# Kernel optimization log

Measured on AMD Instinct MI355X. Metric: run time of the kernel, lower is better.

The kernel has to match this reference:

```python
import jax, jax.numpy as jnp
import numpy as np

RES = 0.16      # config.resolution (m)
XMIN = -51.2    # config.x_min
YMIN = -51.2    # config.y_min
EPS = 1e-5      # BatchNorm eps
NEG = -1.0e9


def setup_inputs() -> dict:
    key = jax.random.key(0)
    ks = jax.random.split(key, 12)
    P, M = 100000, 32
    C_IN, C_MID, C_OUT = 9, 64, 64
    pillars = jax.random.normal(ks[0], (P, M, 4), dtype=jnp.float32)
    pillar_coords = jax.random.randint(ks[1], (P, 2), 0, 640, dtype=jnp.int64)
    num_points_per_pillar = jax.random.randint(ks[2], (P,), 0, 33, dtype=jnp.int64)
    # MLP params (Linear stored as (in,out) for x @ W + b)
    W1 = jax.random.normal(ks[3], (C_IN, C_MID), dtype=jnp.float32) / np.sqrt(C_IN)
    b1 = jax.random.normal(ks[4], (C_MID,), dtype=jnp.float32) * 0.01
    g1 = jnp.ones((C_MID,), jnp.float32)
    beta1 = jnp.zeros((C_MID,), jnp.float32)
    m1 = jax.random.normal(ks[5], (C_MID,), dtype=jnp.float32) * 0.1
    v1 = jax.random.uniform(ks[6], (C_MID,), dtype=jnp.float32, minval=0.5, maxval=1.5)
    W2 = jax.random.normal(ks[7], (C_MID, C_OUT), dtype=jnp.float32) / np.sqrt(C_MID)
    b2 = jax.random.normal(ks[8], (C_OUT,), dtype=jnp.float32) * 0.01
    g2 = jnp.ones((C_OUT,), jnp.float32)
    beta2 = jnp.zeros((C_OUT,), jnp.float32)
    m2 = jax.random.normal(ks[9], (C_OUT,), dtype=jnp.float32) * 0.1
    v2 = jax.random.uniform(ks[10], (C_OUT,), dtype=jnp.float32, minval=0.5, maxval=1.5)
    return {
        "pillars": pillars, "pillar_coords": pillar_coords,
        "num_points_per_pillar": num_points_per_pillar,
        "W1": W1, "b1": b1, "g1": g1, "beta1": beta1, "m1": m1, "v1": v1,
        "W2": W2, "b2": b2, "g2": g2, "beta2": beta2, "m2": m2, "v2": v2,
    }


def reference(pillars, pillar_coords, num_points_per_pillar,
              W1, b1, g1, beta1, m1, v1, W2, b2, g2, beta2, m2, v2):
    P, M, _ = pillars.shape
    # pillar centers from grid indices
    xc = (pillar_coords[:, 1].astype(jnp.float32) + 0.5) * RES + XMIN  # (P,)
    yc = (pillar_coords[:, 0].astype(jnp.float32) + 0.5) * RES + YMIN  # (P,)
    npts = num_points_per_pillar.astype(jnp.float32)
    mask = (jnp.arange(M)[None, :] < num_points_per_pillar[:, None]).astype(pillars.dtype)  # (P,M)
    x, y, z, r = pillars[:, :, 0], pillars[:, :, 1], pillars[:, :, 2], pillars[:, :, 3]
    z_mean = (z * mask).sum(axis=1) / jnp.clip(npts, 1.0)  # (P,)
    xo = x - xc[:, None]
    yo = y - yc[:, None]
    zo = z - z_mean[:, None]
    feat = jnp.stack([x, y, z, r, xo, yo, zo, xo, yo], axis=-1)  # (P,M,9)
    # shared MLP: Linear -> BN(eval) -> ReLU, twice
    h = feat @ W1 + b1
    h = jax.nn.relu(g1 * (h - m1) * jax.lax.rsqrt(v1 + EPS) + beta1)
    h = h @ W2 + b2
    h = jax.nn.relu(g2 * (h - m2) * jax.lax.rsqrt(v2 + EPS) + beta2)  # (P,M,64)
    # masked max over points per pillar
    m3 = mask[:, :, None]
    h = h * m3 + (1.0 - m3) * NEG
    return h.max(axis=1)  # (P,64)
```

## Files before the change

kernel.cpp:

```cpp
#include <hip/hip_runtime.h>
#include <type_traits>

#define RES_ 0.16f
#define XMIN_ -51.2f
#define YMIN_ -51.2f
#define EPS_ 1e-5f
#define NEG_ -1000000000.0f

#define WPB 4

typedef _Float16 f16x8 __attribute__((ext_vector_type(8)));
typedef _Float16 f16x4 __attribute__((ext_vector_type(4)));
typedef _Float16 f16x2 __attribute__((ext_vector_type(2)));
typedef float f32x4 __attribute__((ext_vector_type(4)));

union F8u { f16x8 v; f16x2 h[4]; };
union F4u { f16x4 v; f16x2 h[2]; };

#if __has_builtin(__builtin_amdgcn_mfma_f32_16x16x16f16)
#define MFMA1_K16 1
#else
#define MFMA1_K16 0
#endif

static __device__ __forceinline__ f16x2 pkrtz(float a, float b) {
    return __builtin_bit_cast(f16x2, __builtin_amdgcn_cvt_pkrtz(a, b));
}

static __device__ __forceinline__ f16x2 relu2(f16x2 x) {
#if __has_builtin(__builtin_elementwise_max)
    const f16x2 z2 = (f16x2)(_Float16)0.f;
    return __builtin_elementwise_max(x, z2);
#else
    f16x2 r;
    r[0] = x[0] > (_Float16)0.f ? x[0] : (_Float16)0.f;
    r[1] = x[1] > (_Float16)0.f ? x[1] : (_Float16)0.f;
    return r;
#endif
}

__global__ __launch_bounds__(256, 4) void pfn_kernel(
    const float* __restrict__ pillars,
    const int* __restrict__ coords,
    const int* __restrict__ npts_arr,
    const float* __restrict__ W1, const float* __restrict__ b1,
    const float* __restrict__ g1, const float* __restrict__ beta1,
    const float* __restrict__ m1, const float* __restrict__ v1,
    const float* __restrict__ W2, const float* __restrict__ b2,
    const float* __restrict__ g2, const float* __restrict__ beta2,
    const float* __restrict__ m2, const float* __restrict__ v2,
    float* __restrict__ out, int P)
{
    __shared__ float pts[WPB][32][4];
    __shared__ __align__(16) _Float16 h1s[WPB][32][72];

    const int tid  = threadIdx.x;
    const int wave = tid >> 6;
    const int lane = tid & 63;
    const int quad = lane >> 4;
    const int col  = lane & 15;

    float c1v[4], w16v[4];
#if MFMA1_K16
    f16x4 bw1[4];
#else
    f16x8 bw1[4];
#endif
#pragma unroll
    for (int nt = 0; nt < 4; ++nt) {
        const int n0 = nt * 16 + col;
        const float a1 = g1[n0] * rsqrtf(v1[n0] + EPS_);
        c1v[nt]  = fmaf(a1, b1[n0] - m1[n0], beta1[n0]);
        w16v[nt] = a1 * W1[6 * 64 + n0];
#if MFMA1_K16
#pragma unroll
        for (int j = 0; j < 4; ++j) {
            const int k = quad * 4 + j;
            bw1[nt][j] = (k < 9) ? (_Float16)(a1 * W1[k * 64 + n0]) : (_Float16)0.f;
        }
#else
#pragma unroll
        for (int j = 0; j < 8; ++j) {
            const int k = quad * 8 + j;
            bw1[nt][j] = (k < 9) ? (_Float16)(a1 * W1[k * 64 + n0]) : (_Float16)0.f;
        }
#endif
    }

    f16x8 bw2[2][4];
#pragma unroll
    for (int nt = 0; nt < 4; ++nt) {
        const int n0 = nt * 16 + col;
        const float a2 = g2[n0] * rsqrtf(v2[n0] + EPS_);
#pragma unroll
        for (int kt = 0; kt < 2; ++kt)
#pragma unroll
            for (int j = 0; j < 8; ++j) {
                const int phys = kt * 32 + quad * 8 + j;
                const int orig = (phys & 3) * 16 + (phys >> 2);
                bw2[kt][nt][j] = (_Float16)(a2 * W2[orig * 64 + n0]);
            }
    }
    const float a2o   = g2[lane] * rsqrtf(v2[lane] + EPS_);
    const float c2own = fmaf(a2o, b2[lane] - m2[lane], beta2[lane]);

    const int nwaves = gridDim.x * WPB;
    int p = __builtin_amdgcn_readfirstlane(blockIdx.x * WPB + wave);
    if (p >= P) return;

    float2 pv = ((const float2*)(pillars + (size_t)p * 128))[lane];
    int np = npts_arr[p];
    int cy = coords[2 * p], cx = coords[2 * p + 1];

    while (true) {
        const int pn = p + nwaves;
        const bool has_next = pn < P;
        float2 pvn; int npn = 0, cyn = 0, cxn = 0;
        if (has_next) {
            pvn = ((const float2*)(pillars + (size_t)pn * 128))[lane];
            npn = npts_arr[pn];
            cyn = coords[2 * pn]; cxn = coords[2 * pn + 1];
        }

        np = np < 0 ? 0 : (np > 32 ? 32 : np);
        const int npu = __builtin_amdgcn_readfirstlane(np);
        const float xc = ((float)cx + 0.5f) * RES_ + XMIN_;
        const float yc = ((float)cy + 0.5f) * RES_ + YMIN_;

        ((float2*)&pts[wave][0][0])[lane] = pv;

        float zv = ((lane & 1) && ((lane >> 1) < np)) ? pv.x : 0.0f;
#pragma unroll
        for (int off = 1; off <= 32; off <<= 1) zv += __shfl_xor(zv, off, 64);
        const float z_mean = zv / fmaxf((float)np, 1.0f);

        __threadfence_block();

        auto body = [&](auto MTC) -> float {
            constexpr int MT = decltype(MTC)::value;

#if MFMA1_K16
            f16x4 av1[MT];
#else
            f16x8 av1[MT];
#endif
#pragma unroll
            for (int mt = 0; mt < MT; ++mt) {
                const float4 pt = *(const float4*)&pts[wave][mt * 16 + col][0];
                const float xo = pt.x - xc;
                const float yo = pt.y - yc;
                const f16x2 c01 = pkrtz(pt.x, pt.y);
                const f16x2 c23 = pkrtz(pt.z, pt.w);
                const f16x2 c45 = pkrtz(xo, yo);
                const f16x2 c67 = pkrtz(pt.z, xo);
                const f16x2 c89 = pkrtz(yo, 0.0f);
                const f16x2 z2  = (f16x2)(_Float16)0.f;
#if MFMA1_K16
                F4u u;
                u.h[0] = (quad == 0) ? c01 : (quad == 1) ? c45 : (quad == 2) ? c89 : z2;
                u.h[1] = (quad == 0) ? c23 : (quad == 1) ? c67 : z2;
                av1[mt] = u.v;
#else
                F8u u;
                u.h[0] = (quad == 0) ? c01 : (quad == 1) ? c89 : z2;
                u.h[1] = (quad == 0) ? c23 : z2;
                u.h[2] = (quad == 0) ? c45 : z2;
                u.h[3] = (quad == 0) ? c67 : z2;
                av1[mt] = u.v;
#endif
            }

            f32x4 acc1[MT][4];
#pragma unroll
            for (int nt = 0; nt < 4; ++nt) {
                const float ci = fmaf(-z_mean, w16v[nt], c1v[nt]);
                const f32x4 cinit = {ci, ci, ci, ci};
#pragma unroll
                for (int mt = 0; mt < MT; ++mt)
#if MFMA1_K16
                    acc1[mt][nt] = __builtin_amdgcn_mfma_f32_16x16x16f16(av1[mt], bw1[nt], cinit, 0, 0, 0);
#else
                    acc1[mt][nt] = __builtin_amdgcn_mfma_f32_16x16x32_f16(av1[mt], bw1[nt], cinit, 0, 0, 0);
#endif
            }

#pragma unroll
            for (int mt = 0; mt < MT; ++mt)
#pragma unroll
                for (int r = 0; r < 4; ++r) {
                    const int m = mt * 16 + quad * 4 + r;
                    F4u w;
                    w.h[0] = relu2(pkrtz(acc1[mt][0][r], acc1[mt][1][r]));
                    w.h[1] = relu2(pkrtz(acc1[mt][2][r], acc1[mt][3][r]));
                    *(f16x4*)&h1s[wave][m][col * 4] = w.v;
                }
            __threadfence_block();

            f32x4 acc[MT][4];
            {
                const f32x4 zz = {0.f, 0.f, 0.f, 0.f};
                f16x8 a[MT];
#pragma unroll
                for (int mt = 0; mt < MT; ++mt)
                    a[mt] = *(const f16x8*)&h1s[wave][mt * 16 + col][quad * 8];
#pragma unroll
                for (int nt = 0; nt < 4; ++nt)
#pragma unroll
                    for (int mt = 0; mt < MT; ++mt)
                        acc[mt][nt] = __builtin_amdgcn_mfma_f32_16x16x32_f16(a[mt], bw2[0][nt], zz, 0, 0, 0);
            }
            {
                f16x8 a[MT];
#pragma unroll
                for (int mt = 0; mt < MT; ++mt)
                    a[mt] = *(const f16x8*)&h1s[wave][mt * 16 + col][32 + quad * 8];
#pragma unroll
                for (int nt = 0; nt < 4; ++nt)
#pragma unroll
                    for (int mt = 0; mt < MT; ++mt)
                        acc[mt][nt] = __builtin_amdgcn_mfma_f32_16x16x32_f16(a[mt], bw2[1][nt], acc[mt][nt], 0, 0, 0);
            }

            float hmv[4];
#pragma unroll
            for (int nt = 0; nt < 4; ++nt) {
                float hm = NEG_;
#pragma unroll
                for (int mt = 0; mt < MT; ++mt)
#pragma unroll
                    for (int r = 0; r < 4; ++r) {
                        const int m = mt * 16 + quad * 4 + r;
                        const float val = (m < np) ? acc[mt][nt][r] : NEG_;
                        hm = fmaxf(hm, val);
                    }
                hm = fmaxf(hm, __shfl_xor(hm, 16, 64));
                hm = fmaxf(hm, __shfl_xor(hm, 32, 64));
                hmv[nt] = hm;
            }
            float r0 = (quad == 0) ? hmv[0] : (quad == 1) ? hmv[1] : (quad == 2) ? hmv[2] : hmv[3];
            return fmaxf(r0 + c2own, 0.0f);
        };

        float res;
        if (npu > 16)     res = body(std::integral_constant<int, 2>{});
        else if (npu > 0) res = body(std::integral_constant<int, 1>{});
        else              res = NEG_;
        out[(size_t)p * 64 + lane] = res;

        if (!has_next) break;
        p = pn; pv = pvn; np = npn; cy = cyn; cx = cxn;
    }
}

extern "C" void kernel_launch(void* const* d_in, const int* in_sizes, int n_in,
                              void* d_out, int out_size, void* d_ws, size_t ws_size,
                              hipStream_t stream) {
    const float* pillars = (const float*)d_in[0];
    const int*   coords  = (const int*)d_in[1];
    const int*   npts    = (const int*)d_in[2];
    const float* W1      = (const float*)d_in[3];
    const float* b1      = (const float*)d_in[4];
    const float* g1      = (const float*)d_in[5];
    const float* beta1   = (const float*)d_in[6];
    const float* m1      = (const float*)d_in[7];
    const float* v1      = (const float*)d_in[8];
    const float* W2      = (const float*)d_in[9];
    const float* b2      = (const float*)d_in[10];
    const float* g2      = (const float*)d_in[11];
    const float* beta2   = (const float*)d_in[12];
    const float* m2      = (const float*)d_in[13];
    const float* v2      = (const float*)d_in[14];
    float* out           = (float*)d_out;

    const int P = in_sizes[2];
    const int blocks = 1024;

    hipLaunchKernelGGL(pfn_kernel, dim3(blocks), dim3(256), 0, stream,
                       pillars, coords, npts, W1, b1, g1, beta1, m1, v1,
                       W2, b2, g2, beta2, m2, v2, out, P);
}
```

Measured before the change: 158.9 us.

## Cut accumulator register pressure and fold point mask into MFMA init

Layer-1 MFMAs are now computed in two halves of output tiles, each written to shared memory before the next, and layer-2 accumulates one output tile at a time rather than holding all four. This shrinks live accumulator registers so launch bounds can rise to five blocks per SM, and the grid grows to match. The invalid-point mask is folded into the MFMA accumulator init as a large negative bias, replacing per-element selects before the max. The layer-2 A fragments are loaded once for both K halves, and the tighter register budget could cause spills.

```diff
diff --git a/kernel.cpp b/kernel.cpp
--- a/kernel.cpp
+++ b/kernel.cpp
@@ -39,7 +39,7 @@
 #endif
 }
 
-__global__ __launch_bounds__(256, 4) void pfn_kernel(
+__global__ __launch_bounds__(256, 5) void pfn_kernel(
     const float* __restrict__ pillars,
     const int* __restrict__ coords,
     const int* __restrict__ npts_arr,
@@ -170,69 +170,62 @@
 #endif
             }
 
-            f32x4 acc1[MT][4];
-#pragma unroll
-            for (int nt = 0; nt < 4; ++nt) {
-                const float ci = fmaf(-z_mean, w16v[nt], c1v[nt]);
-                const f32x4 cinit = {ci, ci, ci, ci};
-#pragma unroll
-                for (int mt = 0; mt < MT; ++mt)
-#if MFMA1_K16
-                    acc1[mt][nt] = __builtin_amdgcn_mfma_f32_16x16x16f16(av1[mt], bw1[nt], cinit, 0, 0, 0);
-#else
-                    acc1[mt][nt] = __builtin_amdgcn_mfma_f32_16x16x32_f16(av1[mt], bw1[nt], cinit, 0, 0, 0);
-#endif
-            }
-
-#pragma unroll
-            for (int mt = 0; mt < MT; ++mt)
-#pragma unroll
-                for (int r = 0; r < 4; ++r) {
-                    const int m = mt * 16 + quad * 4 + r;
-                    F4u w;
-                    w.h[0] = relu2(pkrtz(acc1[mt][0][r], acc1[mt][1][r]));
-                    w.h[1] = relu2(pkrtz(acc1[mt][2][r], acc1[mt][3][r]));
-                    *(f16x4*)&h1s[wave][m][col * 4] = w.v;
+#pragma unroll
+            for (int pp = 0; pp < 2; ++pp) {
+                f32x4 acc1[MT][2];
+#pragma unroll
+                for (int ntl = 0; ntl < 2; ++ntl) {
+                    const int nt = pp * 2 + ntl;
+                    const float ci = fmaf(-z_mean, w16v[nt], c1v[nt]);
+                    const f32x4 cinit = {ci, ci, ci, ci};
+#pragma unroll
+                    for (int mt = 0; mt < MT; ++mt)
+#if MFMA1_K16
+                        acc1[mt][ntl] = __builtin_amdgcn_mfma_f32_16x16x16f16(av1[mt], bw1[nt], cinit, 0, 0, 0);
+#else
+                        acc1[mt][ntl] = __builtin_amdgcn_mfma_f32_16x16x32_f16(av1[mt], bw1[nt], cinit, 0, 0, 0);
+#endif
                 }
-            __threadfence_block();
-
-            f32x4 acc[MT][4];
-            {
-                const f32x4 zz = {0.f, 0.f, 0.f, 0.f};
-                f16x8 a[MT];
-#pragma unroll
-                for (int mt = 0; mt < MT; ++mt)
-                    a[mt] = *(const f16x8*)&h1s[wave][mt * 16 + col][quad * 8];
-#pragma unroll
-                for (int nt = 0; nt < 4; ++nt)
-#pragma unroll
-                    for (int mt = 0; mt < MT; ++mt)
-                        acc[mt][nt] = __builtin_amdgcn_mfma_f32_16x16x32_f16(a[mt], bw2[0][nt], zz, 0, 0, 0);
-            }
-            {
-                f16x8 a[MT];
-#pragma unroll
-                for (int mt = 0; mt < MT; ++mt)
-                    a[mt] = *(const f16x8*)&h1s[wave][mt * 16 + col][32 + quad * 8];
-#pragma unroll
-                for (int nt = 0; nt < 4; ++nt)
-#pragma unroll
-                    for (int mt = 0; mt < MT; ++mt)
-                        acc[mt][nt] = __builtin_amdgcn_mfma_f32_16x16x32_f16(a[mt], bw2[1][nt], acc[mt][nt], 0, 0, 0);
-            }
-
-            float hmv[4];
-#pragma unroll
-            for (int nt = 0; nt < 4; ++nt) {
-                float hm = NEG_;
 #pragma unroll
                 for (int mt = 0; mt < MT; ++mt)
 #pragma unroll
                     for (int r = 0; r < 4; ++r) {
                         const int m = mt * 16 + quad * 4 + r;
-                        const float val = (m < np) ? acc[mt][nt][r] : NEG_;
-                        hm = fmaxf(hm, val);
+                        const f16x2 h = relu2(pkrtz(acc1[mt][0][r], acc1[mt][1][r]));
+                        *(f16x2*)&h1s[wave][m][col * 4 + pp * 2] = h;
                     }
+            }
+            __threadfence_block();
+
+            f16x8 a2f[MT][2];
+#pragma unroll
+            for (int mt = 0; mt < MT; ++mt)
+#pragma unroll
+                for (int kt = 0; kt < 2; ++kt)
+                    a2f[mt][kt] = *(const f16x8*)&h1s[wave][mt * 16 + col][kt * 32 + quad * 8];
+
+            f32x4 cm[MT];
+#pragma unroll
+            for (int mt = 0; mt < MT; ++mt)
+#pragma unroll
+                for (int r = 0; r < 4; ++r)
+                    cm[mt][r] = (mt * 16 + quad * 4 + r < np) ? 0.0f : NEG_;
+
+            float hmv[4];
+#pragma unroll
+            for (int nt = 0; nt < 4; ++nt) {
+                f32x4 acc[MT];
+#pragma unroll
+                for (int mt = 0; mt < MT; ++mt) {
+                    acc[mt] = __builtin_amdgcn_mfma_f32_16x16x32_f16(a2f[mt][0], bw2[0][nt], cm[mt], 0, 0, 0);
+                    acc[mt] = __builtin_amdgcn_mfma_f32_16x16x32_f16(a2f[mt][1], bw2[1][nt], acc[mt], 0, 0, 0);
+                }
+                float hm = fmaxf(fmaxf(acc[0][0], acc[0][1]), fmaxf(acc[0][2], acc[0][3]));
+                if (MT == 2) {
+                    const float t1 = fmaxf(fmaxf(acc[MT - 1][0], acc[MT - 1][1]),
+                                           fmaxf(acc[MT - 1][2], acc[MT - 1][3]));
+                    hm = fmaxf(hm, t1);
+                }
                 hm = fmaxf(hm, __shfl_xor(hm, 16, 64));
                 hm = fmaxf(hm, __shfl_xor(hm, 32, 64));
                 hmv[nt] = hm;
@@ -273,7 +266,7 @@
     float* out           = (float*)d_out;
 
     const int P = in_sizes[2];
-    const int blocks = 1024;
+    const int blocks = 1280;
 
     hipLaunchKernelGGL(pfn_kernel, dim3(blocks), dim3(256), 0, stream,
                        pillars, coords, npts, W1, b1, g1, beta1, m1, v1,
```

After: 188.2 us. 1.18x slower.
